# Kernel optimization log

Measured on AMD Instinct MI355X. Metric: run time of the kernel, lower is better.

The kernel has to match this reference:

```python
import jax, jax.numpy as jnp
import numpy as np

N, E = 50000, 1600000
F_IN, C1, H, C2, G, NCLS = 256, 16, 4, 32, 64, 10


def setup_inputs() -> dict:
    ks = jax.random.split(jax.random.key(0), 14)
    x = jax.random.normal(ks[0], (N, F_IN), dtype=jnp.float32)
    edge_index = jax.random.randint(ks[1], (2, E), 0, N, dtype=jnp.int32)
    batch = jnp.sort(jax.random.randint(ks[2], (N,), 0, G, dtype=jnp.int32))
    s1 = 1.0 / np.sqrt(F_IN)
    s2 = 1.0 / np.sqrt(H * C1)
    s3 = 1.0 / np.sqrt(C2)
    return {
        "x": x,
        "edge_index": edge_index,
        "batch": batch,
        "W1": jax.random.normal(ks[3], (F_IN, H * C1), jnp.float32) * s1,
        "att_src1": jax.random.normal(ks[4], (H, C1), jnp.float32) * s2,
        "att_dst1": jax.random.normal(ks[5], (H, C1), jnp.float32) * s2,
        "b1": jnp.zeros((H * C1,), jnp.float32),
        "W2": jax.random.normal(ks[6], (H * C1, C2), jnp.float32) * s2,
        "att_src2": jax.random.normal(ks[7], (1, C2), jnp.float32) * s3,
        "att_dst2": jax.random.normal(ks[8], (1, C2), jnp.float32) * s3,
        "b2": jnp.zeros((C2,), jnp.float32),
        "fc_w": jax.random.normal(ks[9], (C2, NCLS), jnp.float32) * s3,
        "fc_b": jnp.zeros((NCLS,), jnp.float32),
    }


def _gat_conv(x, src, dst, W, a_src, a_dst, b, concat):
    # PyG GATConv: linear per head, LeakyReLU(0.2) edge scores,
    # softmax over incoming edges per destination node, weighted scatter-sum.
    n = x.shape[0]
    heads, ch = a_src.shape
    h = (x @ W).reshape(n, heads, ch)                       # [N, H, C]
    a_s = (h * a_src).sum(-1)                               # [N, H]
    a_d = (h * a_dst).sum(-1)                               # [N, H]
    e = jax.nn.leaky_relu(a_s[src] + a_d[dst], 0.2)         # [E', H]
    m = jax.ops.segment_max(e, dst, num_segments=n)         # [N, H]
    w = jnp.exp(e - m[dst])
    den = jax.ops.segment_sum(w, dst, num_segments=n)
    alpha = w / den[dst]                                    # [E', H]
    out = jax.ops.segment_sum(alpha[:, :, None] * h[src], dst, num_segments=n)
    out = out.reshape(n, heads * ch) if concat else out.mean(axis=1)
    return out + b


def reference(x, edge_index, batch, W1, att_src1, att_dst1, b1,
              W2, att_src2, att_dst2, b2, fc_w, fc_b):
    n = x.shape[0]
    loops = jnp.arange(n, dtype=edge_index.dtype)           # add_self_loops=True
    src = jnp.concatenate([edge_index[0], loops])
    dst = jnp.concatenate([edge_index[1], loops])

    h = jax.nn.elu(_gat_conv(x, src, dst, W1, att_src1, att_dst1, b1, True))
    h = jax.nn.elu(_gat_conv(h, src, dst, W2, att_src2, att_dst2, b2, False))

    # global mean pool over graphs
    sums = jax.ops.segment_sum(h, batch, num_segments=G)    # [G, C2]
    cnt = jax.ops.segment_sum(jnp.ones((n,), h.dtype), batch, num_segments=G)
    pooled = sums / jnp.maximum(cnt, 1.0)[:, None]

    logits = pooled @ fc_w + fc_b
    return jax.nn.log_softmax(logits, axis=1)
```

## Files before the change

kernel.cpp:

```cpp
#include <hip/hip_runtime.h>
#include <hip/hip_bf16.h>

#define GV 64
#define NCLSV 10
#define C2V 32
#define CHUNK 256

using short8 = __attribute__((ext_vector_type(8))) short;
using short4v = __attribute__((ext_vector_type(4))) short;
using f32x4 = __attribute__((ext_vector_type(4))) float;

__device__ __forceinline__ float lrelu(float v) { return v > 0.f ? v : 0.2f * v; }
__device__ __forceinline__ float eluf(float v) { return v > 0.f ? v : expf(v) - 1.f; }

__device__ __forceinline__ unsigned short fbf(float f) {
    unsigned u = __float_as_uint(f);
    u += 0x7fff + ((u >> 16) & 1);
    return (unsigned short)(u >> 16);
}
__device__ __forceinline__ float bff(unsigned short h) {
    return __uint_as_float((unsigned)h << 16);
}

__global__ void zero_kernel(int* p, int n) {
    int i = blockIdx.x * blockDim.x + threadIdx.x;
    if (i < n) p[i] = 0;
}

__global__ void wprep_kernel(const float* __restrict__ W1, const float* __restrict__ W2,
                             short* __restrict__ wt, short* __restrict__ wt2) {
    int t = blockIdx.x * blockDim.x + threadIdx.x;
    for (int e = t; e < 16384; e += gridDim.x * blockDim.x) {
        int k = e >> 6, ch = e & 63;
        wt[ch * 256 + k] = (short)fbf(W1[e]);
    }
    for (int e = t; e < 2048; e += gridDim.x * blockDim.x) {
        int k = e >> 5, ch = e & 31;
        wt2[ch * 64 + k] = (short)fbf(W2[e]);
    }
}

__global__ __launch_bounds__(256) void gemm1_mfma_kernel(
    const float* __restrict__ x, const short* __restrict__ wt,
    const float* __restrict__ as_w, const float* __restrict__ ad_w,
    unsigned short* __restrict__ h1b, float* __restrict__ as1, float* __restrict__ ad1, int N) {
    __shared__ __align__(16) short xs[32 * 256];
    int b0 = blockIdx.x * 32;
    int tid = threadIdx.x;
    #pragma unroll
    for (int i = 0; i < 8; ++i) {
        int e = (tid + i * 256) * 4;
        int node = e >> 8, k = e & 255;
        float4 v = make_float4(0.f, 0.f, 0.f, 0.f);
        if (b0 + node < N) v = *(const float4*)&x[(size_t)(b0 + node) * 256 + k];
        short4v hv;
        hv[0] = (short)fbf(v.x); hv[1] = (short)fbf(v.y);
        hv[2] = (short)fbf(v.z); hv[3] = (short)fbf(v.w);
        int bo = node * 512 + k * 2;
        int sw = bo ^ ((node & 7) << 4);
        *(short4v*)((char*)xs + sw) = hv;
    }
    __syncthreads();
    int w = tid >> 6, lane = tid & 63;
    int ng = w >> 1, cg = w & 1;
    int g = lane >> 4, q = lane & 15;
    int rowb = ng * 16 + q;
    int kb = g * 8;
    f32x4 acc[2];
    acc[0] = (f32x4){0.f, 0.f, 0.f, 0.f};
    acc[1] = (f32x4){0.f, 0.f, 0.f, 0.f};
    #pragma unroll
    for (int ks = 0; ks < 8; ++ks) {
        int kk = ks * 32 + kb;
        int off = (rowb * 512 + kk * 2) ^ ((rowb & 7) << 4);
        short8 a = *(const short8*)((const char*)xs + off);
        #pragma unroll
        for (int ct = 0; ct < 2; ++ct) {
            int ch = cg * 32 + ct * 16 + q;
            short8 b = *(const short8*)(wt + ch * 256 + kk);
            acc[ct] = __builtin_amdgcn_mfma_f32_16x16x32_bf16(a, b, acc[ct], 0, 0, 0);
        }
    }
    #pragma unroll
    for (int ct = 0; ct < 2; ++ct) {
        int chi = cg * 32 + ct * 16 + q;
        float asw = as_w[chi], adw = ad_w[chi];
        int head = cg * 2 + ct;
        #pragma unroll
        for (int r = 0; r < 4; ++r) {
            int node = b0 + ng * 16 + g * 4 + r;
            float val = acc[ct][r];
            if (node < N) h1b[(size_t)node * 64 + chi] = fbf(val);
            float vs = val * asw, vd = val * adw;
            vs += __shfl_xor(vs, 1); vs += __shfl_xor(vs, 2);
            vs += __shfl_xor(vs, 4); vs += __shfl_xor(vs, 8);
            vd += __shfl_xor(vd, 1); vd += __shfl_xor(vd, 2);
            vd += __shfl_xor(vd, 4); vd += __shfl_xor(vd, 8);
            if (q == 0 && node < N) {
                as1[node * 4 + head] = vs;
                ad1[node * 4 + head] = vd;
            }
        }
    }
}

__global__ __launch_bounds__(256) void bucketPre_kernel(
    const int* __restrict__ ei, int E, int EE, int* __restrict__ bcnt,
    int* __restrict__ pbase) {
    __shared__ int hist[256];
    int span = (EE + gridDim.x - 1) / gridDim.x;
    int s0 = blockIdx.x * span;
    int s1 = min(s0 + span, EE);
    hist[threadIdx.x] = 0;
    __syncthreads();
    for (int i = s0 + threadIdx.x; i < s1; i += 256) {
        int d = (i < E) ? ei[E + i] : i - E;
        atomicAdd(&hist[d >> 8], 1);
    }
    __syncthreads();
    int c = hist[threadIdx.x];
    int base = 0;
    if (c) base = atomicAdd(&bcnt[threadIdx.x], c);
    pbase[blockIdx.x * 256 + threadIdx.x] = base;
}

__global__ void bscan_kernel(const int* __restrict__ bcnt, int* __restrict__ bucketoff,
                             int* __restrict__ rowoff, int N, int EE) {
    __shared__ int wtot[4];
    int v = bcnt[threadIdx.x];
    int lane = threadIdx.x & 63, w = threadIdx.x >> 6;
    int inc = v;
    for (int o = 1; o < 64; o <<= 1) { int t = __shfl_up(inc, o); if (lane >= o) inc += t; }
    if (lane == 63) wtot[w] = inc;
    __syncthreads();
    int woff = 0;
    #pragma unroll
    for (int i = 0; i < 4; ++i) woff += (i < w) ? wtot[i] : 0;
    bucketoff[threadIdx.x + 1] = woff + inc;
    if (threadIdx.x == 0) { bucketoff[0] = 0; rowoff[N] = EE; }
}

__global__ __launch_bounds__(256) void bucketA_kernel(
    const int* __restrict__ ei, int E, int EE,
    const int* __restrict__ bucketoff, const int* __restrict__ pbase,
    int* __restrict__ bbuf) {
    __shared__ int base[256];
    __shared__ int cur[256];
    int span = (EE + gridDim.x - 1) / gridDim.x;
    int s0 = blockIdx.x * span;
    int s1 = min(s0 + span, EE);
    if (s0 >= s1) return;
    base[threadIdx.x] = bucketoff[threadIdx.x] + pbase[blockIdx.x * 256 + threadIdx.x];
    cur[threadIdx.x] = 0;
    __syncthreads();
    for (int i = s0 + threadIdx.x; i < s1; i += 256) {
        int s, d;
        if (i < E) { s = ei[i]; d = ei[E + i]; } else { s = d = i - E; }
        int b = d >> 8;
        int lr = atomicAdd(&cur[b], 1);
        bbuf[base[b] + lr] = ((d & 255) << 24) | s;
    }
}

__global__ __launch_bounds__(256) void bucketB_kernel(
    const int* __restrict__ bucketoff, const int* __restrict__ bbuf,
    int* __restrict__ rowoff, int* __restrict__ ssrc, int N) {
    int k = blockIdx.x;
    __shared__ int cnt[256];
    __shared__ int excl[256];
    __shared__ int cur[256];
    __shared__ int wtot[4];
    cnt[threadIdx.x] = 0; cur[threadIdx.x] = 0;
    __syncthreads();
    int lo = bucketoff[k], hi = bucketoff[k + 1];
    for (int i = lo + threadIdx.x; i < hi; i += 256)
        atomicAdd(&cnt[(bbuf[i] >> 24) & 255], 1);
    __syncthreads();
    int v = cnt[threadIdx.x];
    int lane = threadIdx.x & 63, w = threadIdx.x >> 6;
    int inc = v;
    for (int o = 1; o < 64; o <<= 1) { int t = __shfl_up(inc, o); if (lane >= o) inc += t; }
    if (lane == 63) wtot[w] = inc;
    __syncthreads();
    int woff = 0;
    #pragma unroll
    for (int i = 0; i < 4; ++i) woff += (i < w) ? wtot[i] : 0;
    int e = woff + inc - v;
    excl[threadIdx.x] = e;
    int dst = (k << 8) + threadIdx.x;
    if (dst < N) rowoff[dst] = lo + e;
    __syncthreads();
    for (int i = lo + threadIdx.x; i < hi; i += 256) {
        int pv = bbuf[i];
        int dlow = (pv >> 24) & 255;
        int lr = atomicAdd(&cur[dlow], 1);
        ssrc[lo + excl[dlow] + lr] = pv & 0xFFFFFF;
    }
}

__global__ __launch_bounds__(256) void gat1_kernel(
    const int* __restrict__ rowoff, const int* __restrict__ ssrc,
    const float* __restrict__ as1, const float* __restrict__ ad1,
    const unsigned short* __restrict__ h1b, const float* __restrict__ b1,
    unsigned short* __restrict__ h2b, int N) {
    __shared__ int s_s[4][CHUNK];
    __shared__ float s_w[4][4 * CHUNK];
    int wv = threadIdx.x >> 6;
    int lane = threadIdx.x & 63;
    int row = blockIdx.x * 4 + wv;
    if (row >= N) return;
    int beg = rowoff[row], end = rowoff[row + 1];
    int h = lane >> 4, j = lane & 15;
    int par = lane >> 4, cq = lane & 15;
    int hq = cq >> 2;
    float adv = ad1[row * 4 + h];
    float a0c = 0.f, a1c = 0.f, a2c = 0.f, a3c = 0.f;
    float den = 0.f;
    int* sb = s_s[wv];
    float* wb = s_w[wv];
    for (int cb = beg; cb < end; cb += CHUNK) {
        int clen = min(end - cb, CHUNK);
        for (int t = j; t < clen; t += 16) {
            int s = ssrc[cb + t];
            if (h == 0) sb[t] = s;
            float w = __expf(lrelu(as1[s * 4 + h] + adv));
            wb[t * 4 + h] = w;
            den += w;
        }
        int t = par;
        for (; t + 4 < clen; t += 8) {
            int s0 = sb[t], s1 = sb[t + 4];
            float w0 = wb[t * 4 + hq], w1 = wb[(t + 4) * 4 + hq];
            short4v p0 = *(const short4v*)&h1b[(size_t)s0 * 64 + 4 * cq];
            short4v p1 = *(const short4v*)&h1b[(size_t)s1 * 64 + 4 * cq];
            a0c += w0 * bff((unsigned short)p0[0]) + w1 * bff((unsigned short)p1[0]);
            a1c += w0 * bff((unsigned short)p0[1]) + w1 * bff((unsigned short)p1[1]);
            a2c += w0 * bff((unsigned short)p0[2]) + w1 * bff((unsigned short)p1[2]);
            a3c += w0 * bff((unsigned short)p0[3]) + w1 * bff((unsigned short)p1[3]);
        }
        for (; t < clen; t += 4) {
            int s0 = sb[t];
            float w0 = wb[t * 4 + hq];
            short4v p0 = *(const short4v*)&h1b[(size_t)s0 * 64 + 4 * cq];
            a0c += w0 * bff((unsigned short)p0[0]);
            a1c += w0 * bff((unsigned short)p0[1]);
            a2c += w0 * bff((unsigned short)p0[2]);
            a3c += w0 * bff((unsigned short)p0[3]);
        }
    }
    den += __shfl_xor(den, 1);
    den += __shfl_xor(den, 2);
    den += __shfl_xor(den, 4);
    den += __shfl_xor(den, 8);
    float dd = __shfl(den, hq << 4);
    a0c += __shfl_xor(a0c, 16); a0c += __shfl_xor(a0c, 32);
    a1c += __shfl_xor(a1c, 16); a1c += __shfl_xor(a1c, 32);
    a2c += __shfl_xor(a2c, 16); a2c += __shfl_xor(a2c, 32);
    a3c += __shfl_xor(a3c, 16); a3c += __shfl_xor(a3c, 32);
    if (par == 0) {
        float r = 1.f / dd;
        short4v o;
        o[0] = (short)fbf(eluf(a0c * r + b1[4 * cq]));
        o[1] = (short)fbf(eluf(a1c * r + b1[4 * cq + 1]));
        o[2] = (short)fbf(eluf(a2c * r + b1[4 * cq + 2]));
        o[3] = (short)fbf(eluf(a3c * r + b1[4 * cq + 3]));
        *(short4v*)&h2b[(size_t)row * 64 + 4 * cq] = o;
    }
}

__global__ __launch_bounds__(256) void gemm2_mfma_kernel(
    const unsigned short* __restrict__ h2b, const short* __restrict__ wt2,
    const float* __restrict__ as_w, const float* __restrict__ ad_w,
    unsigned short* __restrict__ t2b, float* __restrict__ as2, float* __restrict__ ad2, int N) {
    __shared__ __align__(16) short xs[64 * 64];
    int b0 = blockIdx.x * 64;
    int tid = threadIdx.x;
    #pragma unroll
    for (int i = 0; i < 2; ++i) {
        int e = (tid + i * 256) * 8;
        int node = e >> 6, k = e & 63;
        short8 v = (short8){0, 0, 0, 0, 0, 0, 0, 0};
        if (b0 + node < N) v = *(const short8*)&h2b[(size_t)(b0 + node) * 64 + k];
        int bo = node * 128 + k * 2;
        int sw = bo ^ ((node & 7) << 4);
        *(short8*)((char*)xs + sw) = v;
    }
    __syncthreads();
    int w = tid >> 6, lane = tid & 63;
    int g = lane >> 4, q = lane & 15;
    int rowb = w * 16 + q;
    int kb = g * 8;
    f32x4 acc[2];
    acc[0] = (f32x4){0.f, 0.f, 0.f, 0.f};
    acc[1] = (f32x4){0.f, 0.f, 0.f, 0.f};
    #pragma unroll
    for (int ks = 0; ks < 2; ++ks) {
        int kk = ks * 32 + kb;
        int off = (rowb * 128 + kk * 2) ^ ((rowb & 7) << 4);
        short8 a = *(const short8*)((const char*)xs + off);
        #pragma unroll
        for (int ct = 0; ct < 2; ++ct) {
            int ch = ct * 16 + q;
            short8 b = *(const short8*)(wt2 + ch * 64 + kk);
            acc[ct] = __builtin_amdgcn_mfma_f32_16x16x32_bf16(a, b, acc[ct], 0, 0, 0);
        }
    }
    float asw0 = as_w[q], adw0 = ad_w[q];
    float asw1 = as_w[16 + q], adw1 = ad_w[16 + q];
    #pragma unroll
    for (int r = 0; r < 4; ++r) {
        int node = b0 + w * 16 + g * 4 + r;
        float v0 = acc[0][r], v1 = acc[1][r];
        if (node < N) {
            t2b[(size_t)node * 32 + q] = fbf(v0);
            t2b[(size_t)node * 32 + 16 + q] = fbf(v1);
        }
        float vs = v0 * asw0 + v1 * asw1;
        float vd = v0 * adw0 + v1 * adw1;
        vs += __shfl_xor(vs, 1); vs += __shfl_xor(vs, 2);
        vs += __shfl_xor(vs, 4); vs += __shfl_xor(vs, 8);
        vd += __shfl_xor(vd, 1); vd += __shfl_xor(vd, 2);
        vd += __shfl_xor(vd, 4); vd += __shfl_xor(vd, 8);
        if (q == 0 && node < N) {
            as2[node] = vs;
            ad2[node] = vd;
        }
    }
}

__global__ __launch_bounds__(256) void gat2_kernel(
    const int* __restrict__ rowoff, const int* __restrict__ ssrc,
    const float* __restrict__ as2, const float* __restrict__ ad2,
    const unsigned short* __restrict__ t2b, const float* __restrict__ b2,
    float* __restrict__ h3, int N) {
    __shared__ int s_s[4][CHUNK];
    __shared__ float s_w[4][CHUNK];
    int wv = threadIdx.x >> 6;
    int lane = threadIdx.x & 63;
    int row = blockIdx.x * 4 + wv;
    if (row >= N) return;
    int beg = rowoff[row], end = rowoff[row + 1];
    int par = lane >> 3, cq = lane & 7;
    float adv = ad2[row];
    float a0c = 0.f, a1c = 0.f, a2c = 0.f, a3c = 0.f;
    float den = 0.f;
    int* sb = s_s[wv];
    float* wb = s_w[wv];
    for (int cb = beg; cb < end; cb += CHUNK) {
        int clen = min(end - cb, CHUNK);
        for (int t = lane; t < clen; t += 64) {
            int s = ssrc[cb + t];
            sb[t] = s;
            float w = __expf(lrelu(as2[s] + adv));
            wb[t] = w;
            den += w;
        }
        float c0 = 0.f, c1 = 0.f, c2 = 0.f, c3 = 0.f;
        int t = par;
        for (; t + 8 < clen; t += 16) {
            int s0 = sb[t], s1 = sb[t + 8];
            float w0 = wb[t], w1 = wb[t + 8];
            short4v p0 = *(const short4v*)&t2b[(size_t)s0 * 32 + 4 * cq];
            short4v p1 = *(const short4v*)&t2b[(size_t)s1 * 32 + 4 * cq];
            c0 += w0 * bff((unsigned short)p0[0]) + w1 * bff((unsigned short)p1[0]);
            c1 += w0 * bff((unsigned short)p0[1]) + w1 * bff((unsigned short)p1[1]);
            c2 += w0 * bff((unsigned short)p0[2]) + w1 * bff((unsigned short)p1[2]);
            c3 += w0 * bff((unsigned short)p0[3]) + w1 * bff((unsigned short)p1[3]);
        }
        for (; t < clen; t += 8) {
            int s0 = sb[t];
            float w0 = wb[t];
            short4v p0 = *(const short4v*)&t2b[(size_t)s0 * 32 + 4 * cq];
            c0 += w0 * bff((unsigned short)p0[0]);
            c1 += w0 * bff((unsigned short)p0[1]);
            c2 += w0 * bff((unsigned short)p0[2]);
            c3 += w0 * bff((unsigned short)p0[3]);
        }
        a0c += c0; a1c += c1; a2c += c2; a3c += c3;
    }
    den += __shfl_xor(den, 1);
    den += __shfl_xor(den, 2);
    den += __shfl_xor(den, 4);
    den += __shfl_xor(den, 8);
    den += __shfl_xor(den, 16);
    den += __shfl_xor(den, 32);
    a0c += __shfl_xor(a0c, 8); a0c += __shfl_xor(a0c, 16); a0c += __shfl_xor(a0c, 32);
    a1c += __shfl_xor(a1c, 8); a1c += __shfl_xor(a1c, 16); a1c += __shfl_xor(a1c, 32);
    a2c += __shfl_xor(a2c, 8); a2c += __shfl_xor(a2c, 16); a2c += __shfl_xor(a2c, 32);
    a3c += __shfl_xor(a3c, 8); a3c += __shfl_xor(a3c, 16); a3c += __shfl_xor(a3c, 32);
    if (par == 0) {
        float r = 1.f / den;
        float4 o;
        o.x = eluf(a0c * r + b2[4 * cq]);
        o.y = eluf(a1c * r + b2[4 * cq + 1]);
        o.z = eluf(a2c * r + b2[4 * cq + 2]);
        o.w = eluf(a3c * r + b2[4 * cq + 3]);
        *(float4*)&h3[(size_t)row * 32 + 4 * cq] = o;
    }
}

__device__ __forceinline__ int lowerb(const int* __restrict__ a, int n, int v) {
    int lo = 0, hi = n;
    while (lo < hi) {
        int mid = (lo + hi) >> 1;
        if (a[mid] < v) lo = mid + 1; else hi = mid;
    }
    return lo;
}

__global__ __launch_bounds__(256) void pool_kernel(
    const float* __restrict__ h3, const int* __restrict__ batch,
    float* __restrict__ pooled, float* __restrict__ cnt, int N) {
    int g = blockIdx.x;
    __shared__ int bounds[2];
    if (threadIdx.x == 0) bounds[0] = lowerb(batch, N, g);
    else if (threadIdx.x == 1) bounds[1] = lowerb(batch, N, g + 1);
    __syncthreads();
    int lo = bounds[0], hi = bounds[1];
    int c = threadIdx.x & 31;
    int grp = threadIdx.x >> 5;
    float s = 0.f;
    for (int n = lo + grp; n < hi; n += 8) s += h3[(size_t)n * 32 + c];
    __shared__ float red[8][33];
    red[grp][c] = s;
    __syncthreads();
    if (grp == 0) {
        float t = 0.f;
        for (int k = 0; k < 8; ++k) t += red[k][c];
        pooled[g * C2V + c] = t;
        if (c == 0) cnt[g] = (float)(hi - lo);
    }
}

__global__ void final_kernel(const float* __restrict__ pooled, const float* __restrict__ cnt,
                             const float* __restrict__ fc_w, const float* __restrict__ fc_b,
                             float* __restrict__ out) {
    int g = threadIdx.x;
    if (g >= GV) return;
    float c = cnt[g];
    c = c > 1.f ? c : 1.f;
    float p[C2V];
    for (int j = 0; j < C2V; ++j) p[j] = pooled[g * C2V + j] / c;
    float l[NCLSV];
    float mx = -1e30f;
    for (int k = 0; k < NCLSV; ++k) {
        float acc = fc_b[k];
        for (int j = 0; j < C2V; ++j) acc += p[j] * fc_w[j * NCLSV + k];
        l[k] = acc;
        mx = fmaxf(mx, acc);
    }
    float s = 0.f;
    for (int k = 0; k < NCLSV; ++k) s += expf(l[k] - mx);
    float lse = mx + logf(s);
    for (int k = 0; k < NCLSV; ++k) out[g * NCLSV + k] = l[k] - lse;
}

extern "C" void kernel_launch(void* const* d_in, const int* in_sizes, int n_in,
                              void* d_out, int out_size, void* d_ws, size_t ws_size,
                              hipStream_t stream) {
    const float* x = (const float*)d_in[0];
    const int* ei = (const int*)d_in[1];
    const int* batch = (const int*)d_in[2];
    const float* W1 = (const float*)d_in[3];
    const float* att_src1 = (const float*)d_in[4];
    const float* att_dst1 = (const float*)d_in[5];
    const float* b1 = (const float*)d_in[6];
    const float* W2 = (const float*)d_in[7];
    const float* att_src2 = (const float*)d_in[8];
    const float* att_dst2 = (const float*)d_in[9];
    const float* b2 = (const float*)d_in[10];
    const float* fc_w = (const float*)d_in[11];
    const float* fc_b = (const float*)d_in[12];
    float* out = (float*)d_out;

    int N = in_sizes[0] / 256;
    int E = in_sizes[1] / 2;
    int EE = E + N;
    int NB = (N + 255) >> 8;

    float* ws = (float*)d_ws;
    size_t off = 0;
    int* bcnt = (int*)(ws + off);      off += 256;
    size_t zTot = off;
    int* pbase = (int*)(ws + off);     off += 1024 * 256;
    int* bucketoff = (int*)(ws + off); off += 257;
    float* pooled = ws + off;          off += (size_t)GV * C2V;
    float* cnt = ws + off;             off += (size_t)GV;
    int* rowoff = (int*)(ws + off);    off += (size_t)N + 1;
    int* bbuf = (int*)(ws + off);      off += (size_t)EE;
    int* ssrc = (int*)(ws + off);      off += (size_t)EE;
    short* wt = (short*)(ws + off);    off += 8192;
    short* wt2 = (short*)(ws + off);   off += 1024;
    unsigned short* h1b = (unsigned short*)(ws + off); off += (size_t)32 * N;
    float* as1 = ws + off;             off += (size_t)4 * N;
    float* ad1 = ws + off;             off += (size_t)4 * N;
    unsigned short* h2b = (unsigned short*)(ws + off); off += (size_t)32 * N;
    unsigned short* t2b = (unsigned short*)(ws + off); off += (size_t)16 * N;
    float* as2 = ws + off;             off += (size_t)N;
    float* ad2 = ws + off;             off += (size_t)N;
    float* h3 = ws + off;              off += (size_t)32 * N;

    zero_kernel<<<1, 256, 0, stream>>>((int*)ws, (int)zTot);
    wprep_kernel<<<9, 256, 0, stream>>>(W1, W2, wt, wt2);

    gemm1_mfma_kernel<<<(N + 31) / 32, 256, 0, stream>>>(
        x, wt, att_src1, att_dst1, h1b, as1, ad1, N);

    bucketPre_kernel<<<1024, 256, 0, stream>>>(ei, E, EE, bcnt, pbase);
    bscan_kernel<<<1, 256, 0, stream>>>(bcnt, bucketoff, rowoff, N, EE);
    bucketA_kernel<<<1024, 256, 0, stream>>>(ei, E, EE, bucketoff, pbase, bbuf);
    bucketB_kernel<<<NB, 256, 0, stream>>>(bucketoff, bbuf, rowoff, ssrc, N);

    gat1_kernel<<<(N + 3) / 4, 256, 0, stream>>>(rowoff, ssrc, as1, ad1, h1b, b1, h2b, N);

    gemm2_mfma_kernel<<<(N + 63) / 64, 256, 0, stream>>>(
        h2b, wt2, att_src2, att_dst2, t2b, as2, ad2, N);

    gat2_kernel<<<(N + 3) / 4, 256, 0, stream>>>(rowoff, ssrc, as2, ad2, t2b, b2, h3, N);

    pool_kernel<<<GV, 256, 0, stream>>>(h3, batch, pooled, cnt, N);
    final_kernel<<<1, 64, 0, stream>>>(pooled, cnt, fc_w, fc_b, out);
}
```

Baseline: 218.3 us.

## Split layer-1 features into two head-pair tables and run GAT1 in two passes

Gemm1 now writes the 64-channel layer-1 features as two separate 32-channel bf16 tables, one per head pair, and gat1 runs twice, once per half. The goal is a smaller gather working set per pass (1.6 MB instead of 3.2 MB), which should fit better in L2. Both gat kernels also switch to 16-byte short8 gathers, with each lane handling 8 channels over 16 edge lanes. The cost is reading the edge list and computing exp scores twice, plus one extra launch.

```diff
diff --git a/kernel.cpp b/kernel.cpp
--- a/kernel.cpp
+++ b/kernel.cpp
@@ -43,7 +43,8 @@
 __global__ __launch_bounds__(256) void gemm1_mfma_kernel(
     const float* __restrict__ x, const short* __restrict__ wt,
     const float* __restrict__ as_w, const float* __restrict__ ad_w,
-    unsigned short* __restrict__ h1b, float* __restrict__ as1, float* __restrict__ ad1, int N) {
+    unsigned short* __restrict__ h1lo, unsigned short* __restrict__ h1hi,
+    float* __restrict__ as1, float* __restrict__ ad1, int N) {
     __shared__ __align__(16) short xs[32 * 256];
     int b0 = blockIdx.x * 32;
     int tid = threadIdx.x;
@@ -81,16 +82,18 @@
             acc[ct] = __builtin_amdgcn_mfma_f32_16x16x32_bf16(a, b, acc[ct], 0, 0, 0);
         }
     }
+    unsigned short* dst = cg ? h1hi : h1lo;
     #pragma unroll
     for (int ct = 0; ct < 2; ++ct) {
         int chi = cg * 32 + ct * 16 + q;
+        int ch32 = ct * 16 + q;
         float asw = as_w[chi], adw = ad_w[chi];
         int head = cg * 2 + ct;
         #pragma unroll
         for (int r = 0; r < 4; ++r) {
             int node = b0 + ng * 16 + g * 4 + r;
             float val = acc[ct][r];
-            if (node < N) h1b[(size_t)node * 64 + chi] = fbf(val);
+            if (node < N) dst[(size_t)node * 32 + ch32] = fbf(val);
             float vs = val * asw, vd = val * adw;
             vs += __shfl_xor(vs, 1); vs += __shfl_xor(vs, 2);
             vs += __shfl_xor(vs, 4); vs += __shfl_xor(vs, 8);
@@ -201,70 +204,69 @@
 __global__ __launch_bounds__(256) void gat1_kernel(
     const int* __restrict__ rowoff, const int* __restrict__ ssrc,
     const float* __restrict__ as1, const float* __restrict__ ad1,
-    const unsigned short* __restrict__ h1b, const float* __restrict__ b1,
-    unsigned short* __restrict__ h2b, int N) {
+    const unsigned short* __restrict__ tab, const float* __restrict__ b1,
+    unsigned short* __restrict__ h2b, int N, int ho) {
     __shared__ int s_s[4][CHUNK];
-    __shared__ float s_w[4][4 * CHUNK];
+    __shared__ float s_w[4][2 * CHUNK];
     int wv = threadIdx.x >> 6;
     int lane = threadIdx.x & 63;
     int row = blockIdx.x * 4 + wv;
     if (row >= N) return;
     int beg = rowoff[row], end = rowoff[row + 1];
-    int h = lane >> 4, j = lane & 15;
-    int par = lane >> 4, cq = lane & 15;
-    int hq = cq >> 2;
-    float adv = ad1[row * 4 + h];
-    float a0c = 0.f, a1c = 0.f, a2c = 0.f, a3c = 0.f;
+    int hp = lane >> 5, j = lane & 31;
+    int par = lane >> 2, co = lane & 3;
+    int hq = co >> 1;
+    float adv = ad1[row * 4 + ho + hp];
     float den = 0.f;
+    float a[8];
+    #pragma unroll
+    for (int i = 0; i < 8; ++i) a[i] = 0.f;
     int* sb = s_s[wv];
     float* wb = s_w[wv];
     for (int cb = beg; cb < end; cb += CHUNK) {
         int clen = min(end - cb, CHUNK);
-        for (int t = j; t < clen; t += 16) {
+        for (int t = j; t < clen; t += 32) {
             int s = ssrc[cb + t];
-            if (h == 0) sb[t] = s;
-            float w = __expf(lrelu(as1[s * 4 + h] + adv));
-            wb[t * 4 + h] = w;
+            if (hp == 0) sb[t] = s;
+            float w = __expf(lrelu(as1[s * 4 + ho + hp] + adv));
+            wb[t * 2 + hp] = w;
             den += w;
         }
-        int t = par;
-        for (; t + 4 < clen; t += 8) {
-            int s0 = sb[t], s1 = sb[t + 4];
-            float w0 = wb[t * 4 + hq], w1 = wb[(t + 4) * 4 + hq];
-            short4v p0 = *(const short4v*)&h1b[(size_t)s0 * 64 + 4 * cq];
-            short4v p1 = *(const short4v*)&h1b[(size_t)s1 * 64 + 4 * cq];
-            a0c += w0 * bff((unsigned short)p0[0]) + w1 * bff((unsigned short)p1[0]);
-            a1c += w0 * bff((unsigned short)p0[1]) + w1 * bff((unsigned short)p1[1]);
-            a2c += w0 * bff((unsigned short)p0[2]) + w1 * bff((unsigned short)p1[2]);
-            a3c += w0 * bff((unsigned short)p0[3]) + w1 * bff((unsigned short)p1[3]);
-        }
-        for (; t < clen; t += 4) {
+        for (int t = par; t < clen; t += 16) {
             int s0 = sb[t];
-            float w0 = wb[t * 4 + hq];
-            short4v p0 = *(const short4v*)&h1b[(size_t)s0 * 64 + 4 * cq];
-            a0c += w0 * bff((unsigned short)p0[0]);
-            a1c += w0 * bff((unsigned short)p0[1]);
-            a2c += w0 * bff((unsigned short)p0[2]);
-            a3c += w0 * bff((unsigned short)p0[3]);
+            float w0 = wb[t * 2 + hq];
+            short8 p = *(const short8*)&tab[(size_t)s0 * 32 + 8 * co];
+            a[0] += w0 * bff((unsigned short)p[0]);
+            a[1] += w0 * bff((unsigned short)p[1]);
+            a[2] += w0 * bff((unsigned short)p[2]);
+            a[3] += w0 * bff((unsigned short)p[3]);
+            a[4] += w0 * bff((unsigned short)p[4]);
+            a[5] += w0 * bff((unsigned short)p[5]);
+            a[6] += w0 * bff((unsigned short)p[6]);
+            a[7] += w0 * bff((unsigned short)p[7]);
         }
     }
     den += __shfl_xor(den, 1);
     den += __shfl_xor(den, 2);
     den += __shfl_xor(den, 4);
     den += __shfl_xor(den, 8);
-    float dd = __shfl(den, hq << 4);
-    a0c += __shfl_xor(a0c, 16); a0c += __shfl_xor(a0c, 32);
-    a1c += __shfl_xor(a1c, 16); a1c += __shfl_xor(a1c, 32);
-    a2c += __shfl_xor(a2c, 16); a2c += __shfl_xor(a2c, 32);
-    a3c += __shfl_xor(a3c, 16); a3c += __shfl_xor(a3c, 32);
+    den += __shfl_xor(den, 16);
+    float dd = __shfl(den, hq << 5);
+    #pragma unroll
+    for (int i = 0; i < 8; ++i) {
+        a[i] += __shfl_xor(a[i], 4);
+        a[i] += __shfl_xor(a[i], 8);
+        a[i] += __shfl_xor(a[i], 16);
+        a[i] += __shfl_xor(a[i], 32);
+    }
     if (par == 0) {
         float r = 1.f / dd;
-        short4v o;
-        o[0] = (short)fbf(eluf(a0c * r + b1[4 * cq]));
-        o[1] = (short)fbf(eluf(a1c * r + b1[4 * cq + 1]));
-        o[2] = (short)fbf(eluf(a2c * r + b1[4 * cq + 2]));
-        o[3] = (short)fbf(eluf(a3c * r + b1[4 * cq + 3]));
-        *(short4v*)&h2b[(size_t)row * 64 + 4 * cq] = o;
+        int cbase = (ho >> 1) * 32 + 8 * co;
+        short8 o;
+        #pragma unroll
+        for (int i = 0; i < 8; ++i)
+            o[i] = (short)fbf(eluf(a[i] * r + b1[cbase + i]));
+        *(short8*)&h2b[(size_t)row * 64 + cbase] = o;
     }
 }
 
@@ -340,10 +342,12 @@
     int row = blockIdx.x * 4 + wv;
     if (row >= N) return;
     int beg = rowoff[row], end = rowoff[row + 1];
-    int par = lane >> 3, cq = lane & 7;
+    int par = lane >> 2, co = lane & 3;
     float adv = ad2[row];
-    float a0c = 0.f, a1c = 0.f, a2c = 0.f, a3c = 0.f;
     float den = 0.f;
+    float a[8];
+    #pragma unroll
+    for (int i = 0; i < 8; ++i) a[i] = 0.f;
     int* sb = s_s[wv];
     float* wb = s_w[wv];
     for (int cb = beg; cb < end; cb += CHUNK) {
@@ -355,28 +359,19 @@
             wb[t] = w;
             den += w;
         }
-        float c0 = 0.f, c1 = 0.f, c2 = 0.f, c3 = 0.f;
-        int t = par;
-        for (; t + 8 < clen; t += 16) {
-            int s0 = sb[t], s1 = sb[t + 8];
-            float w0 = wb[t], w1 = wb[t + 8];
-            short4v p0 = *(const short4v*)&t2b[(size_t)s0 * 32 + 4 * cq];
-            short4v p1 = *(const short4v*)&t2b[(size_t)s1 * 32 + 4 * cq];
-            c0 += w0 * bff((unsigned short)p0[0]) + w1 * bff((unsigned short)p1[0]);
-            c1 += w0 * bff((unsigned short)p0[1]) + w1 * bff((unsigned short)p1[1]);
-            c2 += w0 * bff((unsigned short)p0[2]) + w1 * bff((unsigned short)p1[2]);
-            c3 += w0 * bff((unsigned short)p0[3]) + w1 * bff((unsigned short)p1[3]);
-        }
-        for (; t < clen; t += 8) {
+        for (int t = par; t < clen; t += 16) {
             int s0 = sb[t];
             float w0 = wb[t];
-            short4v p0 = *(const short4v*)&t2b[(size_t)s0 * 32 + 4 * cq];
-            c0 += w0 * bff((unsigned short)p0[0]);
-            c1 += w0 * bff((unsigned short)p0[1]);
-            c2 += w0 * bff((unsigned short)p0[2]);
-            c3 += w0 * bff((unsigned short)p0[3]);
-        }
-        a0c += c0; a1c += c1; a2c += c2; a3c += c3;
+            short8 p = *(const short8*)&t2b[(size_t)s0 * 32 + 8 * co];
+            a[0] += w0 * bff((unsigned short)p[0]);
+            a[1] += w0 * bff((unsigned short)p[1]);
+            a[2] += w0 * bff((unsigned short)p[2]);
+            a[3] += w0 * bff((unsigned short)p[3]);
+            a[4] += w0 * bff((unsigned short)p[4]);
+            a[5] += w0 * bff((unsigned short)p[5]);
+            a[6] += w0 * bff((unsigned short)p[6]);
+            a[7] += w0 * bff((unsigned short)p[7]);
+        }
     }
     den += __shfl_xor(den, 1);
     den += __shfl_xor(den, 2);
@@ -384,18 +379,26 @@
     den += __shfl_xor(den, 8);
     den += __shfl_xor(den, 16);
     den += __shfl_xor(den, 32);
-    a0c += __shfl_xor(a0c, 8); a0c += __shfl_xor(a0c, 16); a0c += __shfl_xor(a0c, 32);
-    a1c += __shfl_xor(a1c, 8); a1c += __shfl_xor(a1c, 16); a1c += __shfl_xor(a1c, 32);
-    a2c += __shfl_xor(a2c, 8); a2c += __shfl_xor(a2c, 16); a2c += __shfl_xor(a2c, 32);
-    a3c += __shfl_xor(a3c, 8); a3c += __shfl_xor(a3c, 16); a3c += __shfl_xor(a3c, 32);
+    #pragma unroll
+    for (int i = 0; i < 8; ++i) {
+        a[i] += __shfl_xor(a[i], 4);
+        a[i] += __shfl_xor(a[i], 8);
+        a[i] += __shfl_xor(a[i], 16);
+        a[i] += __shfl_xor(a[i], 32);
+    }
     if (par == 0) {
         float r = 1.f / den;
-        float4 o;
-        o.x = eluf(a0c * r + b2[4 * cq]);
-        o.y = eluf(a1c * r + b2[4 * cq + 1]);
-        o.z = eluf(a2c * r + b2[4 * cq + 2]);
-        o.w = eluf(a3c * r + b2[4 * cq + 3]);
-        *(float4*)&h3[(size_t)row * 32 + 4 * cq] = o;
+        float4 o0, o1;
+        o0.x = eluf(a[0] * r + b2[8 * co]);
+        o0.y = eluf(a[1] * r + b2[8 * co + 1]);
+        o0.z = eluf(a[2] * r + b2[8 * co + 2]);
+        o0.w = eluf(a[3] * r + b2[8 * co + 3]);
+        o1.x = eluf(a[4] * r + b2[8 * co + 4]);
+        o1.y = eluf(a[5] * r + b2[8 * co + 5]);
+        o1.z = eluf(a[6] * r + b2[8 * co + 6]);
+        o1.w = eluf(a[7] * r + b2[8 * co + 7]);
+        *(float4*)&h3[(size_t)row * 32 + 8 * co] = o0;
+        *(float4*)&h3[(size_t)row * 32 + 8 * co + 4] = o1;
     }
 }
 
@@ -491,7 +494,8 @@
     int* ssrc = (int*)(ws + off);      off += (size_t)EE;
     short* wt = (short*)(ws + off);    off += 8192;
     short* wt2 = (short*)(ws + off);   off += 1024;
-    unsigned short* h1b = (unsigned short*)(ws + off); off += (size_t)32 * N;
+    unsigned short* h1lo = (unsigned short*)(ws + off); off += (size_t)16 * N;
+    unsigned short* h1hi = (unsigned short*)(ws + off); off += (size_t)16 * N;
     float* as1 = ws + off;             off += (size_t)4 * N;
     float* ad1 = ws + off;             off += (size_t)4 * N;
     unsigned short* h2b = (unsigned short*)(ws + off); off += (size_t)32 * N;
@@ -504,14 +508,15 @@
     wprep_kernel<<<9, 256, 0, stream>>>(W1, W2, wt, wt2);
 
     gemm1_mfma_kernel<<<(N + 31) / 32, 256, 0, stream>>>(
-        x, wt, att_src1, att_dst1, h1b, as1, ad1, N);
+        x, wt, att_src1, att_dst1, h1lo, h1hi, as1, ad1, N);
 
     bucketPre_kernel<<<1024, 256, 0, stream>>>(ei, E, EE, bcnt, pbase);
     bscan_kernel<<<1, 256, 0, stream>>>(bcnt, bucketoff, rowoff, N, EE);
     bucketA_kernel<<<1024, 256, 0, stream>>>(ei, E, EE, bucketoff, pbase, bbuf);
     bucketB_kernel<<<NB, 256, 0, stream>>>(bucketoff, bbuf, rowoff, ssrc, N);
 
-    gat1_kernel<<<(N + 3) / 4, 256, 0, stream>>>(rowoff, ssrc, as1, ad1, h1b, b1, h2b, N);
+    gat1_kernel<<<(N + 3) / 4, 256, 0, stream>>>(rowoff, ssrc, as1, ad1, h1lo, b1, h2b, N, 0);
+    gat1_kernel<<<(N + 3) / 4, 256, 0, stream>>>(rowoff, ssrc, as1, ad1, h1hi, b1, h2b, N, 2);
 
     gemm2_mfma_kernel<<<(N + 63) / 64, 256, 0, stream>>>(
         h2b, wt2, att_src2, att_dst2, t2b, as2, ad2, N);
```

New measurement: 246.7 us. 13.0% more time.

## Fuse edge-weight and gather in gat2 with 16-byte loads, drop LDS staging

Applied to the files above, without the earlier changes.

The layer-2 aggregation kernel now computes each edge weight and gathers the neighbour's features in a single pass. It no longer stages source indices and weights in shared memory first. Each lane handles 8 bf16 channels with a 16-byte load, and 16 edges are processed in parallel per wavefront instead of 8. Workspace offsets are rounded to 16-byte alignment so the vector loads and stores stay aligned. In exchange, each weight is computed redundantly by 4 lanes, and more exp and attention-score loads are issued per edge.

```diff
diff --git a/kernel.cpp b/kernel.cpp
--- a/kernel.cpp
+++ b/kernel.cpp
@@ -333,69 +333,55 @@
     const float* __restrict__ as2, const float* __restrict__ ad2,
     const unsigned short* __restrict__ t2b, const float* __restrict__ b2,
     float* __restrict__ h3, int N) {
-    __shared__ int s_s[4][CHUNK];
-    __shared__ float s_w[4][CHUNK];
     int wv = threadIdx.x >> 6;
     int lane = threadIdx.x & 63;
     int row = blockIdx.x * 4 + wv;
     if (row >= N) return;
     int beg = rowoff[row], end = rowoff[row + 1];
-    int par = lane >> 3, cq = lane & 7;
+    int par = lane >> 2, co = lane & 3;
     float adv = ad2[row];
-    float a0c = 0.f, a1c = 0.f, a2c = 0.f, a3c = 0.f;
     float den = 0.f;
-    int* sb = s_s[wv];
-    float* wb = s_w[wv];
-    for (int cb = beg; cb < end; cb += CHUNK) {
-        int clen = min(end - cb, CHUNK);
-        for (int t = lane; t < clen; t += 64) {
-            int s = ssrc[cb + t];
-            sb[t] = s;
-            float w = __expf(lrelu(as2[s] + adv));
-            wb[t] = w;
-            den += w;
-        }
-        float c0 = 0.f, c1 = 0.f, c2 = 0.f, c3 = 0.f;
-        int t = par;
-        for (; t + 8 < clen; t += 16) {
-            int s0 = sb[t], s1 = sb[t + 8];
-            float w0 = wb[t], w1 = wb[t + 8];
-            short4v p0 = *(const short4v*)&t2b[(size_t)s0 * 32 + 4 * cq];
-            short4v p1 = *(const short4v*)&t2b[(size_t)s1 * 32 + 4 * cq];
-            c0 += w0 * bff((unsigned short)p0[0]) + w1 * bff((unsigned short)p1[0]);
-            c1 += w0 * bff((unsigned short)p0[1]) + w1 * bff((unsigned short)p1[1]);
-            c2 += w0 * bff((unsigned short)p0[2]) + w1 * bff((unsigned short)p1[2]);
-            c3 += w0 * bff((unsigned short)p0[3]) + w1 * bff((unsigned short)p1[3]);
-        }
-        for (; t < clen; t += 8) {
-            int s0 = sb[t];
-            float w0 = wb[t];
-            short4v p0 = *(const short4v*)&t2b[(size_t)s0 * 32 + 4 * cq];
-            c0 += w0 * bff((unsigned short)p0[0]);
-            c1 += w0 * bff((unsigned short)p0[1]);
-            c2 += w0 * bff((unsigned short)p0[2]);
-            c3 += w0 * bff((unsigned short)p0[3]);
-        }
-        a0c += c0; a1c += c1; a2c += c2; a3c += c3;
-    }
-    den += __shfl_xor(den, 1);
-    den += __shfl_xor(den, 2);
+    float a[8];
+    #pragma unroll
+    for (int i = 0; i < 8; ++i) a[i] = 0.f;
+    for (int t = beg + par; t < end; t += 16) {
+        int s0 = ssrc[t];
+        float w = __expf(lrelu(as2[s0] + adv));
+        den += w;
+        short8 p = *(const short8*)&t2b[(size_t)s0 * 32 + 8 * co];
+        a[0] += w * bff((unsigned short)p[0]);
+        a[1] += w * bff((unsigned short)p[1]);
+        a[2] += w * bff((unsigned short)p[2]);
+        a[3] += w * bff((unsigned short)p[3]);
+        a[4] += w * bff((unsigned short)p[4]);
+        a[5] += w * bff((unsigned short)p[5]);
+        a[6] += w * bff((unsigned short)p[6]);
+        a[7] += w * bff((unsigned short)p[7]);
+    }
     den += __shfl_xor(den, 4);
     den += __shfl_xor(den, 8);
     den += __shfl_xor(den, 16);
     den += __shfl_xor(den, 32);
-    a0c += __shfl_xor(a0c, 8); a0c += __shfl_xor(a0c, 16); a0c += __shfl_xor(a0c, 32);
-    a1c += __shfl_xor(a1c, 8); a1c += __shfl_xor(a1c, 16); a1c += __shfl_xor(a1c, 32);
-    a2c += __shfl_xor(a2c, 8); a2c += __shfl_xor(a2c, 16); a2c += __shfl_xor(a2c, 32);
-    a3c += __shfl_xor(a3c, 8); a3c += __shfl_xor(a3c, 16); a3c += __shfl_xor(a3c, 32);
+    #pragma unroll
+    for (int i = 0; i < 8; ++i) {
+        a[i] += __shfl_xor(a[i], 4);
+        a[i] += __shfl_xor(a[i], 8);
+        a[i] += __shfl_xor(a[i], 16);
+        a[i] += __shfl_xor(a[i], 32);
+    }
     if (par == 0) {
         float r = 1.f / den;
-        float4 o;
-        o.x = eluf(a0c * r + b2[4 * cq]);
-        o.y = eluf(a1c * r + b2[4 * cq + 1]);
-        o.z = eluf(a2c * r + b2[4 * cq + 2]);
-        o.w = eluf(a3c * r + b2[4 * cq + 3]);
-        *(float4*)&h3[(size_t)row * 32 + 4 * cq] = o;
+        float4 o0, o1;
+        o0.x = eluf(a[0] * r + b2[8 * co]);
+        o0.y = eluf(a[1] * r + b2[8 * co + 1]);
+        o0.z = eluf(a[2] * r + b2[8 * co + 2]);
+        o0.w = eluf(a[3] * r + b2[8 * co + 3]);
+        o1.x = eluf(a[4] * r + b2[8 * co + 4]);
+        o1.y = eluf(a[5] * r + b2[8 * co + 5]);
+        o1.z = eluf(a[6] * r + b2[8 * co + 6]);
+        o1.w = eluf(a[7] * r + b2[8 * co + 7]);
+        *(float4*)&h3[(size_t)row * 32 + 8 * co] = o0;
+        *(float4*)&h3[(size_t)row * 32 + 8 * co + 4] = o1;
     }
 }
 
@@ -484,9 +470,11 @@
     size_t zTot = off;
     int* pbase = (int*)(ws + off);     off += 1024 * 256;
     int* bucketoff = (int*)(ws + off); off += 257;
+    off = (off + 3) & ~(size_t)3;
     float* pooled = ws + off;          off += (size_t)GV * C2V;
     float* cnt = ws + off;             off += (size_t)GV;
     int* rowoff = (int*)(ws + off);    off += (size_t)N + 1;
+    off = (off + 3) & ~(size_t)3;
     int* bbuf = (int*)(ws + off);      off += (size_t)EE;
     int* ssrc = (int*)(ws + off);      off += (size_t)EE;
     short* wt = (short*)(ws + off);    off += 8192;
@@ -498,6 +486,7 @@
     unsigned short* t2b = (unsigned short*)(ws + off); off += (size_t)16 * N;
     float* as2 = ws + off;             off += (size_t)N;
     float* ad2 = ws + off;             off += (size_t)N;
+    off = (off + 3) & ~(size_t)3;
     float* h3 = ws + off;              off += (size_t)32 * N;
 
     zero_kernel<<<1, 256, 0, stream>>>((int*)ws, (int)zTot);
```

New measurement: 219.9 us. Within noise of the previous version (+0.7%).
